# Kernel tuning notes

Hardware: AMD Instinct MI355X
Metric: run time of the kernel (lower is better)

The kernel has to match this reference:

```python
import jax, jax.numpy as jnp
import numpy as np

N = 100000   # nodes
E = 800000   # edges
P = 100000   # pos/neg pairs
H = 4        # heads
IN = 128     # input feature dim
HID = 32     # per-head out dim (H*HID = 128)


def gat_layer(h, src, dst, W, al, ar, b):
    """DGL-style GATConv: gather -> leaky_relu attention -> segment softmax -> scatter."""
    n = h.shape[0]
    nh, nf = al.shape
    feat = (h @ W).reshape(n, nh, nf)                       # [N,H,F]
    el = jnp.einsum('nhf,hf->nh', feat, al)                 # [N,H]
    er = jnp.einsum('nhf,hf->nh', feat, ar)                 # [N,H]
    e = jax.nn.leaky_relu(el[src] + er[dst], negative_slope=0.2)  # [E,H]
    emax = jax.ops.segment_max(e, dst, num_segments=n)      # [N,H]
    emax = jnp.where(jnp.isfinite(emax), emax, 0.0)         # zero-in-degree guard
    w = jnp.exp(e - emax[dst])                              # [E,H]
    denom = jax.ops.segment_sum(w, dst, num_segments=n)     # [N,H]
    alpha = w / jnp.maximum(denom[dst], 1e-9)               # [E,H]
    out = jax.ops.segment_sum(feat[src] * alpha[:, :, None], dst, num_segments=n)  # [N,H,F]
    return out.reshape(n, nh * nf) + b


def setup_inputs() -> dict:
    key = jax.random.key(0)
    ks = jax.random.split(key, 32)
    s = 0.1
    d = {
        'x': jax.random.normal(ks[0], (N, IN), jnp.float32),
        'src': jax.random.randint(ks[1], (E,), 0, N),
        'dst': jax.random.randint(ks[2], (E,), 0, N),
        'pos_src': jax.random.randint(ks[3], (P,), 0, N),
        'pos_dst': jax.random.randint(ks[4], (P,), 0, N),
        'neg_src': jax.random.randint(ks[5], (P,), 0, N),
        'neg_dst': jax.random.randint(ks[6], (P,), 0, N),
    }
    HF = H * HID
    # 3 GATConv layers, all 128 -> 4x32
    for l in range(3):
        ind = IN if l == 0 else HF
        d[f'W{l}'] = s * jax.random.normal(ks[7 + 4 * l], (ind, HF), jnp.float32)
        d[f'al{l}'] = s * jax.random.normal(ks[8 + 4 * l], (H, HID), jnp.float32)
        d[f'ar{l}'] = s * jax.random.normal(ks[9 + 4 * l], (H, HID), jnp.float32)
        d[f'b{l}'] = jnp.zeros((HF,), jnp.float32)
    # projection 128 -> 32
    d['Wp'] = s * jax.random.normal(ks[20], (HF, HID), jnp.float32)
    d['bp'] = jnp.zeros((HID,), jnp.float32)
    # predictor MLP 32 -> 32 -> 32 -> 1
    d['Wq1'] = s * jax.random.normal(ks[21], (HID, HID), jnp.float32)
    d['bq1'] = jnp.zeros((HID,), jnp.float32)
    d['Wq2'] = s * jax.random.normal(ks[22], (HID, HID), jnp.float32)
    d['bq2'] = jnp.zeros((HID,), jnp.float32)
    d['Wq3'] = s * jax.random.normal(ks[23], (HID, 1), jnp.float32)
    d['bq3'] = jnp.zeros((1,), jnp.float32)
    return d


def reference(x, src, dst, pos_src, pos_dst, neg_src, neg_dst,
              W0, al0, ar0, b0, W1, al1, ar1, b1, W2, al2, ar2, b2,
              Wp, bp, Wq1, bq1, Wq2, bq2, Wq3, bq3):
    h = x
    for W, al, ar, b in ((W0, al0, ar0, b0), (W1, al1, ar1, b1), (W2, al2, ar2, b2)):
        h = jax.nn.elu(gat_layer(h, src, dst, W, al, ar, b))
    h = h @ Wp + bp                                          # [N,HID]

    def predictor(z):
        z = jax.nn.relu(z @ Wq1 + bq1)
        z = jax.nn.relu(z @ Wq2 + bq2)
        return z @ Wq3 + bq3

    h_pos = predictor(h[pos_src] * h[pos_dst])               # [P,1]
    h_neg = predictor(h[neg_src] * h[neg_dst])               # [P,1]
    return (h_pos, h_neg)
```

## Files before the change

### kernel.cpp

```cpp
#include <hip/hip_runtime.h>
#include <math.h>

typedef __attribute__((ext_vector_type(8))) short bf16x8;
typedef __attribute__((ext_vector_type(4))) float f32x4;

__device__ __forceinline__ unsigned short f2bf_rtne(float v) {
    unsigned u = __float_as_uint(v);
    u += 0x7FFFu + ((u >> 16) & 1u);
    return (unsigned short)(u >> 16);
}

__global__ __launch_bounds__(256) void hist_k(const int* __restrict__ dst, int* __restrict__ deg, int e) {
    int i = blockIdx.x * 256 + threadIdx.x;
    if (i < e) atomicAdd(&deg[dst[i]], 1);
}

__global__ __launch_bounds__(256) void scan1_k(const int* __restrict__ deg, int* __restrict__ rowptr,
                                               int* __restrict__ bsum, int n) {
    __shared__ int sh[256];
    int tid = threadIdx.x;
    int sid = blockIdx.x * 256 + tid;
    int v = (sid < n) ? deg[sid] : 0;
    sh[tid] = v; __syncthreads();
    for (int off = 1; off < 256; off <<= 1) {
        int t = (tid >= off) ? sh[tid - off] : 0;
        __syncthreads();
        sh[tid] += t;
        __syncthreads();
    }
    if (sid < n) rowptr[sid + 1] = sh[tid];
    if (tid == 255) bsum[blockIdx.x] = sh[255];
}

__global__ __launch_bounds__(512) void scan2_k(int* __restrict__ bsum, int nb) {
    __shared__ int sh[512];
    int tid = threadIdx.x;
    sh[tid] = (tid < nb) ? bsum[tid] : 0;
    __syncthreads();
    for (int off = 1; off < 512; off <<= 1) {
        int t = (tid >= off) ? sh[tid - off] : 0;
        __syncthreads();
        sh[tid] += t;
        __syncthreads();
    }
    if (tid < nb) bsum[tid] = sh[tid];
}

__global__ __launch_bounds__(256) void scan3_k(int* __restrict__ rowptr, const int* __restrict__ bsum, int n) {
    int sid = blockIdx.x * 256 + threadIdx.x;
    if (sid == 0) rowptr[0] = 0;
    if (sid < n && blockIdx.x > 0) rowptr[sid + 1] += bsum[blockIdx.x - 1];
}

__global__ __launch_bounds__(256) void fill_k(const int* __restrict__ src, const int* __restrict__ dst,
                                              const int* __restrict__ rowptr, int* __restrict__ cursor,
                                              int* __restrict__ csrc, int* __restrict__ cdst, int e) {
    int i = blockIdx.x * 256 + threadIdx.x;
    if (i < e) {
        int d = dst[i];
        int pos = rowptr[d] + atomicAdd(&cursor[d], 1);
        csrc[pos] = src[i];
        cdst[pos] = d;
    }
}

__global__ __launch_bounds__(256) void wconv_k(const float* __restrict__ W,
                                               unsigned short* __restrict__ Wth,
                                               unsigned short* __restrict__ Wtl) {
    int idx = blockIdx.x * 256 + threadIdx.x;
    int k = idx >> 7, n = idx & 127;
    float v = W[idx];
    unsigned short h = f2bf_rtne(v);
    float hf = __uint_as_float((unsigned)h << 16);
    Wth[n * 128 + k] = h;
    Wtl[n * 128 + k] = f2bf_rtne(v - hf);
}

__global__ __launch_bounds__(256) void gemm_mfma_k(const float* __restrict__ A,
        const unsigned short* __restrict__ Wth, const unsigned short* __restrict__ Wtl,
        const float* __restrict__ alp, const float* __restrict__ arp,
        float* __restrict__ C, float* __restrict__ el, float* __restrict__ er, int M) {
    int tid = threadIdx.x;
    int wv = tid >> 6, lane = tid & 63;
    int l15 = lane & 15, lhi = lane >> 4;
    int mb = blockIdx.x * 128 + wv * 32;

    f32x4 acc[2][8];
    #pragma unroll
    for (int f = 0; f < 2; f++)
        #pragma unroll
        for (int n = 0; n < 8; n++) acc[f][n] = (f32x4){0.f, 0.f, 0.f, 0.f};

    float alv[8], arv[8];
    #pragma unroll
    for (int n = 0; n < 8; n++) { alv[n] = alp[n * 16 + l15]; arv[n] = arp[n * 16 + l15]; }

    int r0 = mb + l15, r1 = mb + 16 + l15;
    const float* a0p = A + (size_t)min(r0, M - 1) * 128 + lhi * 8;
    const float* a1p = A + (size_t)min(r1, M - 1) * 128 + lhi * 8;

    #pragma unroll
    for (int ks = 0; ks < 4; ks++) {
        int kb = ks * 32 + lhi * 8;
        float av[8];
        bf16x8 a0h, a0l, a1h, a1l;
        *(float4*)(av)     = *(const float4*)(a0p + ks * 32);
        *(float4*)(av + 4) = *(const float4*)(a0p + ks * 32 + 4);
        #pragma unroll
        for (int j = 0; j < 8; j++) {
            unsigned short h = f2bf_rtne(av[j]);
            a0h[j] = (short)h;
            a0l[j] = (short)f2bf_rtne(av[j] - __uint_as_float((unsigned)h << 16));
        }
        *(float4*)(av)     = *(const float4*)(a1p + ks * 32);
        *(float4*)(av + 4) = *(const float4*)(a1p + ks * 32 + 4);
        #pragma unroll
        for (int j = 0; j < 8; j++) {
            unsigned short h = f2bf_rtne(av[j]);
            a1h[j] = (short)h;
            a1l[j] = (short)f2bf_rtne(av[j] - __uint_as_float((unsigned)h << 16));
        }
        #pragma unroll
        for (int n = 0; n < 8; n++) {
            bf16x8 bhv = *(const bf16x8*)(Wth + (size_t)(n * 16 + l15) * 128 + kb);
            bf16x8 blv = *(const bf16x8*)(Wtl + (size_t)(n * 16 + l15) * 128 + kb);
            acc[0][n] = __builtin_amdgcn_mfma_f32_16x16x32_bf16(a0h, bhv, acc[0][n], 0, 0, 0);
            acc[1][n] = __builtin_amdgcn_mfma_f32_16x16x32_bf16(a1h, bhv, acc[1][n], 0, 0, 0);
            acc[0][n] = __builtin_amdgcn_mfma_f32_16x16x32_bf16(a0l, bhv, acc[0][n], 0, 0, 0);
            acc[1][n] = __builtin_amdgcn_mfma_f32_16x16x32_bf16(a1l, bhv, acc[1][n], 0, 0, 0);
            acc[0][n] = __builtin_amdgcn_mfma_f32_16x16x32_bf16(a0h, blv, acc[0][n], 0, 0, 0);
            acc[1][n] = __builtin_amdgcn_mfma_f32_16x16x32_bf16(a1h, blv, acc[1][n], 0, 0, 0);
        }
    }

    #pragma unroll
    for (int f = 0; f < 2; f++) {
        #pragma unroll
        for (int i = 0; i < 4; i++) {
            int r = mb + f * 16 + lhi * 4 + i;
            bool ok = (r < M);
            if (ok) {
                #pragma unroll
                for (int n = 0; n < 8; n++)
                    C[(size_t)r * 128 + n * 16 + l15] = acc[f][n][i];
            }
            float ph[4], qh[4];
            #pragma unroll
            for (int h = 0; h < 4; h++) {
                ph[h] = acc[f][2 * h][i] * alv[2 * h] + acc[f][2 * h + 1][i] * alv[2 * h + 1];
                qh[h] = acc[f][2 * h][i] * arv[2 * h] + acc[f][2 * h + 1][i] * arv[2 * h + 1];
            }
            #pragma unroll
            for (int off = 1; off < 16; off <<= 1) {
                #pragma unroll
                for (int h = 0; h < 4; h++) {
                    ph[h] += __shfl_xor(ph[h], off);
                    qh[h] += __shfl_xor(qh[h], off);
                }
            }
            if (ok && l15 < 8) {
                if (l15 < 4) {
                    float v = (l15 == 0) ? ph[0] : (l15 == 1) ? ph[1] : (l15 == 2) ? ph[2] : ph[3];
                    el[(size_t)r * 4 + l15] = v;
                } else {
                    int h = l15 - 4;
                    float v = (h == 0) ? qh[0] : (h == 1) ? qh[1] : (h == 2) ? qh[2] : qh[3];
                    er[(size_t)r * 4 + h] = v;
                }
            }
        }
    }
}

__global__ __launch_bounds__(256) void edgew_k(const int* __restrict__ csrc, const int* __restrict__ cdst,
                                               const float* __restrict__ el, const float* __restrict__ er,
                                               float* __restrict__ wbuf, int e) {
    int p = blockIdx.x * 256 + threadIdx.x;
    if (p >= e) return;
    int s = csrc[p], d = cdst[p];
    float4 l4 = *(const float4*)(el + (size_t)s * 4);
    float4 r4 = *(const float4*)(er + (size_t)d * 4);
    float e0 = l4.x + r4.x, e1 = l4.y + r4.y, e2 = l4.z + r4.z, e3 = l4.w + r4.w;
    e0 = (e0 > 0.f) ? e0 : 0.2f * e0;
    e1 = (e1 > 0.f) ? e1 : 0.2f * e1;
    e2 = (e2 > 0.f) ? e2 : 0.2f * e2;
    e3 = (e3 > 0.f) ? e3 : 0.2f * e3;
    *(float4*)(wbuf + (size_t)p * 4) = make_float4(__expf(e0), __expf(e1), __expf(e2), __expf(e3));
}

__global__ __launch_bounds__(256) void aggregate_k(const float* __restrict__ feat, const float* __restrict__ wbuf,
                                                   const int* __restrict__ rowptr, const int* __restrict__ csrc,
                                                   const float* __restrict__ bias, float* __restrict__ out, int n) {
    int wid = threadIdx.x >> 6;
    int lane = threadIdx.x & 63;
    int node = blockIdx.x * 4 + wid;
    if (node >= n) return;
    int h = lane >> 4;
    int p0 = rowptr[node], p1 = rowptr[node + 1];
    float2 b2 = *(const float2*)(bias + lane * 2);
    float lsum = 0.f, a0 = 0.f, a1 = 0.f;
    int p = p0;
    for (; p + 4 <= p1; p += 4) {
        int s0 = csrc[p], s1 = csrc[p + 1], s2 = csrc[p + 2], s3 = csrc[p + 3];
        float w0 = wbuf[(size_t)p * 4 + h];
        float w1 = wbuf[(size_t)(p + 1) * 4 + h];
        float w2 = wbuf[(size_t)(p + 2) * 4 + h];
        float w3 = wbuf[(size_t)(p + 3) * 4 + h];
        float2 f0 = *(const float2*)(feat + (size_t)s0 * 128 + lane * 2);
        float2 f1 = *(const float2*)(feat + (size_t)s1 * 128 + lane * 2);
        float2 f2 = *(const float2*)(feat + (size_t)s2 * 128 + lane * 2);
        float2 f3 = *(const float2*)(feat + (size_t)s3 * 128 + lane * 2);
        lsum += (w0 + w1) + (w2 + w3);
        a0 += w0 * f0.x + w1 * f1.x + w2 * f2.x + w3 * f3.x;
        a1 += w0 * f0.y + w1 * f1.y + w2 * f2.y + w3 * f3.y;
    }
    for (; p < p1; ++p) {
        int s = csrc[p];
        float w = wbuf[(size_t)p * 4 + h];
        float2 f = *(const float2*)(feat + (size_t)s * 128 + lane * 2);
        lsum += w;
        a0 += w * f.x;
        a1 += w * f.y;
    }
    float inv = 1.f / fmaxf(lsum, 1e-9f);
    float v0 = a0 * inv + b2.x;
    float v1 = a1 * inv + b2.y;
    v0 = (v0 > 0.f) ? v0 : expm1f(v0);
    v1 = (v1 > 0.f) ? v1 : expm1f(v1);
    *(float2*)(out + (size_t)node * 128 + lane * 2) = make_float2(v0, v1);
}

__global__ __launch_bounds__(256) void proj_k(const float* __restrict__ h, const float* __restrict__ Wp,
                                              const float* __restrict__ bp, float* __restrict__ hp, int n) {
    __shared__ float Ws[128 * 32];
    __shared__ float Hs[32][132];
    int tid = threadIdx.x;
    for (int i = tid; i < 4096; i += 256) Ws[i] = Wp[i];
    int n0 = blockIdx.x * 32;
    for (int i = tid; i < 1024; i += 256) {
        int r = i >> 5, c4 = i & 31;
        int node = n0 + r;
        float4 v = (node < n) ? *(const float4*)(h + (size_t)node * 128 + c4 * 4)
                              : make_float4(0.f, 0.f, 0.f, 0.f);
        *(float4*)&Hs[r][c4 * 4] = v;
    }
    __syncthreads();
    int r = tid >> 3;
    int node = n0 + r;
    int j0 = (tid & 7) * 4;
    if (node < n) {
        float a0 = bp[j0], a1 = bp[j0 + 1], a2 = bp[j0 + 2], a3 = bp[j0 + 3];
        #pragma unroll
        for (int k = 0; k < 128; k++) {
            float av = Hs[r][k];
            float4 w = *(const float4*)&Ws[k * 32 + j0];
            a0 += av * w.x; a1 += av * w.y; a2 += av * w.z; a3 += av * w.w;
        }
        *(float4*)(hp + (size_t)node * 32 + j0) = make_float4(a0, a1, a2, a3);
    }
}

__global__ __launch_bounds__(256) void predictor_k(const float* __restrict__ hp,
                                                   const int* __restrict__ ps, const int* __restrict__ pd,
                                                   const int* __restrict__ ns, const int* __restrict__ nd,
                                                   const float* __restrict__ Wq1, const float* __restrict__ bq1,
                                                   const float* __restrict__ Wq2, const float* __restrict__ bq2,
                                                   const float* __restrict__ Wq3, const float* __restrict__ bq3,
                                                   float* __restrict__ out, int P) {
    __shared__ float w1[1024], w2[1024], w3[32], b1[32], b2[32];
    int tid = threadIdx.x;
    for (int i = tid; i < 1024; i += 256) { w1[i] = Wq1[i]; w2[i] = Wq2[i]; }
    if (tid < 32) { w3[tid] = Wq3[tid]; b1[tid] = bq1[tid]; b2[tid] = bq2[tid]; }
    __syncthreads();
    int gid = blockIdx.x * 256 + tid;
    if (gid >= 2 * P) return;
    int i = (gid < P) ? gid : gid - P;
    int a = (gid < P) ? ps[i] : ns[i];
    int b = (gid < P) ? pd[i] : nd[i];
    float z[32];
    const float4* ha = (const float4*)(hp + (size_t)a * 32);
    const float4* hb = (const float4*)(hp + (size_t)b * 32);
    #pragma unroll
    for (int q = 0; q < 8; q++) {
        float4 x = ha[q], y = hb[q];
        z[q * 4 + 0] = x.x * y.x; z[q * 4 + 1] = x.y * y.y;
        z[q * 4 + 2] = x.z * y.z; z[q * 4 + 3] = x.w * y.w;
    }
    float z1[32];
    #pragma unroll
    for (int j = 0; j < 32; j++) {
        float s = b1[j];
        #pragma unroll
        for (int k = 0; k < 32; k++) s += z[k] * w1[k * 32 + j];
        z1[j] = fmaxf(s, 0.f);
    }
    #pragma unroll
    for (int j = 0; j < 32; j++) {
        float s = b2[j];
        #pragma unroll
        for (int k = 0; k < 32; k++) s += z1[k] * w2[k * 32 + j];
        z[j] = fmaxf(s, 0.f);
    }
    float s3 = bq3[0];
    #pragma unroll
    for (int j = 0; j < 32; j++) s3 += z[j] * w3[j];
    out[gid] = s3;
}

extern "C" void kernel_launch(void* const* d_in, const int* in_sizes, int n_in,
                              void* d_out, int out_size, void* d_ws, size_t ws_size,
                              hipStream_t stream) {
    const float* x   = (const float*)d_in[0];
    const int* src   = (const int*)d_in[1];
    const int* dst   = (const int*)d_in[2];
    const int* psrc  = (const int*)d_in[3];
    const int* pdst  = (const int*)d_in[4];
    const int* nsrc  = (const int*)d_in[5];
    const int* ndst  = (const int*)d_in[6];
    const float* W[3]  = { (const float*)d_in[7],  (const float*)d_in[11], (const float*)d_in[15] };
    const float* al[3] = { (const float*)d_in[8],  (const float*)d_in[12], (const float*)d_in[16] };
    const float* ar[3] = { (const float*)d_in[9],  (const float*)d_in[13], (const float*)d_in[17] };
    const float* bb[3] = { (const float*)d_in[10], (const float*)d_in[14], (const float*)d_in[18] };
    const float* Wp  = (const float*)d_in[19];
    const float* bp  = (const float*)d_in[20];
    const float* Wq1 = (const float*)d_in[21];
    const float* bq1 = (const float*)d_in[22];
    const float* Wq2 = (const float*)d_in[23];
    const float* bq2 = (const float*)d_in[24];
    const float* Wq3 = (const float*)d_in[25];
    const float* bq3 = (const float*)d_in[26];
    float* out = (float*)d_out;

    const int N = in_sizes[0] / 128;
    const int E = in_sizes[1];
    const int P = in_sizes[3];

    size_t off = 0;
    auto alloc = [&](size_t bytes) {
        void* p = (char*)d_ws + off;
        off += (bytes + 255) & ~(size_t)255;
        return p;
    };
    float* bufF  = (float*)alloc((size_t)N * 128 * 4);
    float* bufH  = (float*)alloc((size_t)N * 128 * 4);
    float* elA   = (float*)alloc((size_t)N * 4 * 4);
    float* erA   = (float*)alloc((size_t)N * 4 * 4);
    float* hp    = (float*)alloc((size_t)N * 32 * 4);
    int* rowptr  = (int*)alloc((size_t)(N + 1) * 4);
    int* csrc    = (int*)alloc((size_t)E * 4);
    int* cdst    = (int*)alloc((size_t)E * 4);
    float* wbuf  = (float*)alloc((size_t)E * 4 * 4);
    int* deg     = (int*)alloc((size_t)N * 4);
    int* cursor  = (int*)alloc((size_t)N * 4);
    int* bsum    = (int*)alloc(1024 * 4);
    unsigned short* Wth = (unsigned short*)alloc(16384 * 2);
    unsigned short* Wtl = (unsigned short*)alloc(16384 * 2);
    (void)ws_size;

    const int NB_E = (E + 255) / 256;
    const int NB_N = (N + 255) / 256;

    hipMemsetAsync(deg, 0, (size_t)N * 4, stream);
    hipMemsetAsync(cursor, 0, (size_t)N * 4, stream);

    hist_k<<<NB_E, 256, 0, stream>>>(dst, deg, E);
    scan1_k<<<NB_N, 256, 0, stream>>>(deg, rowptr, bsum, N);
    scan2_k<<<1, 512, 0, stream>>>(bsum, NB_N);
    scan3_k<<<NB_N, 256, 0, stream>>>(rowptr, bsum, N);
    fill_k<<<NB_E, 256, 0, stream>>>(src, dst, rowptr, cursor, csrc, cdst, E);

    const int GEMM_B = (N + 127) / 128;
    const float* hin = x;
    for (int l = 0; l < 3; l++) {
        wconv_k<<<64, 256, 0, stream>>>(W[l], Wth, Wtl);
        gemm_mfma_k<<<GEMM_B, 256, 0, stream>>>(hin, Wth, Wtl, al[l], ar[l], bufF, elA, erA, N);
        edgew_k<<<NB_E, 256, 0, stream>>>(csrc, cdst, elA, erA, wbuf, E);
        aggregate_k<<<(N + 3) / 4, 256, 0, stream>>>(bufF, wbuf, rowptr, csrc, bb[l], bufH, N);
        hin = bufH;
    }
    proj_k<<<(N + 31) / 32, 256, 0, stream>>>(bufH, Wp, bp, hp, N);
    predictor_k<<<(2 * P + 255) / 256, 256, 0, stream>>>(hp, psrc, pdst, nsrc, ndst,
                                                         Wq1, bq1, Wq2, bq2, Wq3, bq3, out, P);
}
```

Measured before the change: 557.5 us.

## Pre-pack weights into MFMA fragment layout and stage via double-buffered LDS

The weight conversion kernel now writes hi/lo bf16 weights in a packed per-lane MFMA fragment order. The GEMM kernel stages each k-slice of that packed buffer into shared memory with a two-buffer ping-pong, and every wave reads its B fragments from LDS with contiguous per-lane 16-byte loads. Before, each wave loaded strided fragments straight from global memory. This adds per-k-step barriers and 32KB of LDS per block, which may reduce occupancy. The GEMM is only part of the total time, which is dominated by the edge kernels.

```diff
diff --git a/kernel.cpp b/kernel.cpp
--- a/kernel.cpp
+++ b/kernel.cpp
@@ -64,22 +64,24 @@
     }
 }
 
-__global__ __launch_bounds__(256) void wconv_k(const float* __restrict__ W,
-                                               unsigned short* __restrict__ Wth,
-                                               unsigned short* __restrict__ Wtl) {
+__global__ __launch_bounds__(256) void wconv_k(const float* __restrict__ W, unsigned short* __restrict__ Bp) {
     int idx = blockIdx.x * 256 + threadIdx.x;
-    int k = idx >> 7, n = idx & 127;
+    int k = idx >> 7, nc = idx & 127;
     float v = W[idx];
     unsigned short h = f2bf_rtne(v);
     float hf = __uint_as_float((unsigned)h << 16);
-    Wth[n * 128 + k] = h;
-    Wtl[n * 128 + k] = f2bf_rtne(v - hf);
+    unsigned short lo = f2bf_rtne(v - hf);
+    int n = nc >> 4, l15 = nc & 15, ks = k >> 5, lhi = (k >> 3) & 3, j = k & 7;
+    int lanei = lhi * 16 + l15;
+    Bp[(((ks * 16 + 2 * n) * 64) + lanei) * 8 + j] = h;
+    Bp[(((ks * 16 + 2 * n + 1) * 64) + lanei) * 8 + j] = lo;
 }
 
 __global__ __launch_bounds__(256) void gemm_mfma_k(const float* __restrict__ A,
-        const unsigned short* __restrict__ Wth, const unsigned short* __restrict__ Wtl,
+        const unsigned short* __restrict__ Bp,
         const float* __restrict__ alp, const float* __restrict__ arp,
         float* __restrict__ C, float* __restrict__ el, float* __restrict__ er, int M) {
+    __shared__ short Bs[2][16][64][8];
     int tid = threadIdx.x;
     int wv = tid >> 6, lane = tid & 63;
     int l15 = lane & 15, lhi = lane >> 4;
@@ -95,13 +97,26 @@
     #pragma unroll
     for (int n = 0; n < 8; n++) { alv[n] = alp[n * 16 + l15]; arv[n] = arp[n * 16 + l15]; }
 
-    int r0 = mb + l15, r1 = mb + 16 + l15;
-    const float* a0p = A + (size_t)min(r0, M - 1) * 128 + lhi * 8;
-    const float* a1p = A + (size_t)min(r1, M - 1) * 128 + lhi * 8;
+    const float* a0p = A + (size_t)min(mb + l15, M - 1) * 128 + lhi * 8;
+    const float* a1p = A + (size_t)min(mb + 16 + l15, M - 1) * 128 + lhi * 8;
+
+    {
+        const float4* g = (const float4*)Bp;
+        float4* s = (float4*)&Bs[0][0][0][0];
+        #pragma unroll
+        for (int p = 0; p < 4; p++) s[tid + p * 256] = g[tid + p * 256];
+    }
 
     #pragma unroll
     for (int ks = 0; ks < 4; ks++) {
-        int kb = ks * 32 + lhi * 8;
+        int buf = ks & 1;
+        __syncthreads();
+        if (ks < 3) {
+            const float4* g = (const float4*)Bp + (size_t)(ks + 1) * 1024;
+            float4* s = (float4*)&Bs[buf ^ 1][0][0][0];
+            #pragma unroll
+            for (int p = 0; p < 4; p++) s[tid + p * 256] = g[tid + p * 256];
+        }
         float av[8];
         bf16x8 a0h, a0l, a1h, a1l;
         *(float4*)(av)     = *(const float4*)(a0p + ks * 32);
@@ -120,10 +135,11 @@
             a1h[j] = (short)h;
             a1l[j] = (short)f2bf_rtne(av[j] - __uint_as_float((unsigned)h << 16));
         }
+        const bf16x8* bsv = (const bf16x8*)&Bs[buf][0][0][0];
         #pragma unroll
         for (int n = 0; n < 8; n++) {
-            bf16x8 bhv = *(const bf16x8*)(Wth + (size_t)(n * 16 + l15) * 128 + kb);
-            bf16x8 blv = *(const bf16x8*)(Wtl + (size_t)(n * 16 + l15) * 128 + kb);
+            bf16x8 bhv = bsv[(2 * n) * 64 + lane];
+            bf16x8 blv = bsv[(2 * n + 1) * 64 + lane];
             acc[0][n] = __builtin_amdgcn_mfma_f32_16x16x32_bf16(a0h, bhv, acc[0][n], 0, 0, 0);
             acc[1][n] = __builtin_amdgcn_mfma_f32_16x16x32_bf16(a1h, bhv, acc[1][n], 0, 0, 0);
             acc[0][n] = __builtin_amdgcn_mfma_f32_16x16x32_bf16(a0l, bhv, acc[0][n], 0, 0, 0);
@@ -353,8 +369,7 @@
     int* deg     = (int*)alloc((size_t)N * 4);
     int* cursor  = (int*)alloc((size_t)N * 4);
     int* bsum    = (int*)alloc(1024 * 4);
-    unsigned short* Wth = (unsigned short*)alloc(16384 * 2);
-    unsigned short* Wtl = (unsigned short*)alloc(16384 * 2);
+    unsigned short* Bp = (unsigned short*)alloc(32768 * 2);
     (void)ws_size;
 
     const int NB_E = (E + 255) / 256;
@@ -372,8 +387,8 @@
     const int GEMM_B = (N + 127) / 128;
     const float* hin = x;
     for (int l = 0; l < 3; l++) {
-        wconv_k<<<64, 256, 0, stream>>>(W[l], Wth, Wtl);
-        gemm_mfma_k<<<GEMM_B, 256, 0, stream>>>(hin, Wth, Wtl, al[l], ar[l], bufF, elA, erA, N);
+        wconv_k<<<64, 256, 0, stream>>>(W[l], Bp);
+        gemm_mfma_k<<<GEMM_B, 256, 0, stream>>>(hin, Bp, al[l], ar[l], bufF, elA, erA, N);
         edgew_k<<<NB_E, 256, 0, stream>>>(csrc, cdst, elA, erA, wbuf, E);
         aggregate_k<<<(N + 3) / 4, 256, 0, stream>>>(bufF, wbuf, rowptr, csrc, bb[l], bufH, N);
         hin = bufH;
```

New measurement: 507.6 us. 1.1x faster.
